# Optimization experiments

Hardware: AMD Instinct MI355X
Metric: run time of the kernel (lower is better)

Reference implementation:

```python
import jax, jax.numpy as jnp
import numpy as np
import math

DIM_K = 64  # head dim used for scaling
NEG = -1000000000.0

def setup_inputs() -> dict:
    key = jax.random.key(0)
    k1, k2, k3, k4 = jax.random.split(key, 4)
    B, H, S, D = 4, 16, 2048, 64
    return {
        "key": jax.random.normal(k1, (B, H, S, D), dtype=jnp.float32),
        "query": jax.random.normal(k2, (B, H, S, D), dtype=jnp.float32),
        "value": jax.random.normal(k3, (B, H, S, D), dtype=jnp.float32),
        "mask": jax.random.randint(k4, (B, S, S), 0, 2, dtype=jnp.int32),
    }

def reference(key, query, value, mask):
    # scores: [B,H,Sq,Sk]
    scores = jnp.einsum('bhqd,bhkd->bhqk', query, key) / math.sqrt(DIM_K)
    scores = jnp.where(mask[:, None, :, :] == 0, NEG, scores)
    attn = jax.nn.softmax(scores, axis=-1)  # dropout is identity in eval mode
    return jnp.einsum('bhqk,bhkd->bhqd', attn, value)
```

## Files before the change

kernel.cpp:

```cpp
#include <hip/hip_runtime.h>
#include <hip/hip_bf16.h>
#include <stdint.h>

#define B_ 4
#define H_ 16
#define S_ 2048
#define D_ 64
#define NKT (S_ / 64)
#define QM 128

typedef __attribute__((ext_vector_type(8))) short bf16x8;
typedef __attribute__((ext_vector_type(4))) float f32x4;
typedef unsigned long long u64;
typedef unsigned int u32;

__device__ inline short f2bf(float f) {
  union { float f; u32 u; } x; x.f = f;
  u32 r = x.u + 0x7FFFu + ((x.u >> 16) & 1u);
  return (short)(r >> 16);
}
__device__ inline short4 f2bf4(float4 v) {
  short4 s; s.x = f2bf(v.x); s.y = f2bf(v.y); s.z = f2bf(v.z); s.w = f2bf(v.w);
  return s;
}

__device__ inline int SW(int row, int byteoff) {
  return row * 128 + (byteoff ^ ((row & 7) << 4));
}

__device__ inline void gll16(const void* g, void* l) {
  __builtin_amdgcn_global_load_lds(
      (const __attribute__((address_space(1))) u32*)g,
      (__attribute__((address_space(3))) u32*)(uintptr_t)l, 16, 0, 0);
}

__global__ __launch_bounds__(256)
void prepass(const float* __restrict__ Kg, const float* __restrict__ Vg,
             const int* __restrict__ Mg,
             char* __restrict__ Ksw, char* __restrict__ Vsw, u64* __restrict__ Mp) {
  __shared__ short tile[4096];
  const int bid = blockIdx.x, tid = threadIdx.x;
  if (bid < 8192) {
    int idx = bid * 256 + tid;
    int row = idx >> 4, c4 = idx & 15;
    float4 v = *(const float4*)(Kg + (size_t)idx * 4);
    *(short4*)(Ksw + (size_t)row * 128 + ((c4 * 8) ^ ((row & 7) << 4))) = f2bf4(v);
  } else if (bid < 10240) {
    int vb = bid - 8192;
    char* ct = (char*)tile;
    int c4 = tid & 15, g = tid >> 4;
    const float* src = Vg + (size_t)vb * (64 * D_) + (size_t)(g * 4) * D_ + c4 * 4;
    float4 vv[4];
#pragma unroll
    for (int i = 0; i < 4; ++i) vv[i] = *(const float4*)(src + (size_t)i * D_);
    const float* vf = (const float*)vv;
#pragma unroll
    for (int dd = 0; dd < 4; ++dd) {
      short4 s;
      s.x = f2bf(vf[0 * 4 + dd]);
      s.y = f2bf(vf[1 * 4 + dd]);
      s.z = f2bf(vf[2 * 4 + dd]);
      s.w = f2bf(vf[3 * 4 + dd]);
      *(short4*)(ct + SW(c4 * 4 + dd, g * 8)) = s;
    }
    __syncthreads();
    char* dst = Vsw + (size_t)vb * 8192;
#pragma unroll
    for (int j = 0; j < 2; ++j)
      *(float4*)(dst + tid * 16 + j * 4096) = *(const float4*)(ct + tid * 16 + j * 4096);
  } else {
    int pb = bid - 10240;
    int gbase = pb * 1024;
#pragma unroll
    for (int j = 0; j < 4; ++j) {
      int idx = gbase + j * 256 + tid;
      u64 bits = __ballot(Mg[idx] != 0);
      if ((tid & 63) == 0) Mp[idx >> 6] = bits;
    }
  }
}

__global__ __launch_bounds__(256, 4)
void attn_kernel(const float* __restrict__ Qg,
                 const char* __restrict__ Ksw,
                 const char* __restrict__ Vsw,
                 const u64* __restrict__ Mp,
                 float* __restrict__ Og) {
  __shared__ short sK[2][4096];
  __shared__ short sV[2][4096];

  const int tid  = threadIdx.x;
  const int w    = tid >> 6;
  const int lane = tid & 63;
  const int quad = lane >> 4;
  const int c    = lane & 15;
  const int bh   = blockIdx.y;
  const int b    = bh >> 4;
  const int q0   = blockIdx.x * QM;
  const size_t base = (size_t)bh * (S_ * D_);
  const char* Kt = Ksw + (size_t)bh * (S_ * 128);
  const char* Vt = Vsw + (size_t)bh * (S_ * 128);
  char* cK0 = (char*)sK;

  const float SC = 0.125f * 1.44269504088896f;
#pragma unroll
  for (int j = 0; j < 8; ++j) {
    int idx = tid + j * 256;
    int row = idx >> 4, c4 = idx & 15;
    float4 v = *(const float4*)(Qg + base + (size_t)(q0 + row) * D_ + c4 * 4);
    v.x *= SC; v.y *= SC; v.z *= SC; v.w *= SC;
    *(short4*)(cK0 + SW(row, c4 * 8)) = f2bf4(v);
  }
  __syncthreads();
  bf16x8 qa[2][2];
#pragma unroll
  for (int gi = 0; gi < 2; ++gi) {
    qa[gi][0] = *(bf16x8*)(cK0 + SW(32 * w + 16 * gi + c, quad * 16));
    qa[gi][1] = *(bf16x8*)(cK0 + SW(32 * w + 16 * gi + c, 64 + quad * 16));
  }
  __syncthreads();

#pragma unroll
  for (int j = 0; j < 2; ++j) {
    gll16(Kt + tid * 16 + j * 4096, (char*)sK[0] + tid * 16 + j * 4096);
    gll16(Vt + tid * 16 + j * 4096, (char*)sV[0] + tid * 16 + j * 4096);
  }

  f32x4 acco[2][4];
  float l_part[2] = {0.f, 0.f};
#pragma unroll
  for (int gi = 0; gi < 2; ++gi)
#pragma unroll
    for (int i = 0; i < 4; ++i) acco[gi][i] = f32x4{0, 0, 0, 0};

  const u64* mrowp = Mp + ((size_t)b * S_ + q0 + 32 * w + c) * NKT;

  for (int kt = 0; kt < NKT; ++kt) {
    const char* cK = (const char*)sK[kt & 1];
    const char* cV = (const char*)sV[kt & 1];

    __syncthreads();

    u64 mw[2];
    mw[0] = mrowp[kt];
    mw[1] = mrowp[16 * NKT + kt];

    f32x4 accs[2][4];
#pragma unroll
    for (int n = 0; n < 4; ++n) {
      bf16x8 kb0 = *(bf16x8*)(cK + SW(16 * n + c, quad * 16));
      bf16x8 kb1 = *(bf16x8*)(cK + SW(16 * n + c, 64 + quad * 16));
#pragma unroll
      for (int gi = 0; gi < 2; ++gi) {
        f32x4 z = {0, 0, 0, 0};
        z = __builtin_amdgcn_mfma_f32_16x16x32_bf16(kb0, qa[gi][0], z, 0, 0, 0);
        z = __builtin_amdgcn_mfma_f32_16x16x32_bf16(kb1, qa[gi][1], z, 0, 0, 0);
        accs[gi][n] = z;
      }
    }

    if (kt + 1 < NKT) {
      char* kn = (char*)sK[(kt + 1) & 1];
      char* vn = (char*)sV[(kt + 1) & 1];
      const char* kg = Kt + (size_t)(kt + 1) * 8192;
      const char* vg = Vt + (size_t)(kt + 1) * 8192;
#pragma unroll
      for (int j = 0; j < 2; ++j) {
        gll16(kg + tid * 16 + j * 4096, kn + tid * 16 + j * 4096);
        gll16(vg + tid * 16 + j * 4096, vn + tid * 16 + j * 4096);
      }
    }

    bf16x8 pa[2][2];
#pragma unroll
    for (int gi = 0; gi < 2; ++gi) {
      u32 mlo = (u32)(mw[gi] >> (4 * quad));
      u32 mhi = (u32)(mw[gi] >> (4 * quad + 32));
      float e[4][4];
#pragma unroll
      for (int n = 0; n < 4; ++n) {
        u32 mword = (n < 2) ? mlo : mhi;
        int sh = 16 * (n & 1);
#pragma unroll
        for (int r = 0; r < 4; ++r)
          e[n][r] = ((mword >> (sh + r)) & 1u) ? exp2f(accs[gi][n][r]) : 0.0f;
      }
      l_part[gi] += ((e[0][0] + e[0][1]) + (e[0][2] + e[0][3]))
                  + ((e[1][0] + e[1][1]) + (e[1][2] + e[1][3]))
                  + ((e[2][0] + e[2][1]) + (e[2][2] + e[2][3]))
                  + ((e[3][0] + e[3][1]) + (e[3][2] + e[3][3]));

      u32 pk[4][2];
#pragma unroll
      for (int n = 0; n < 4; ++n) {
        union { __hip_bfloat162 h; u32 u; } p0, p1;
        p0.h = __float22bfloat162_rn(make_float2(e[n][0], e[n][1]));
        p1.h = __float22bfloat162_rn(make_float2(e[n][2], e[n][3]));
        pk[n][0] = p0.u;
        pk[n][1] = p1.u;
      }

#pragma unroll
      for (int t = 0; t < 2; ++t) {
        union { bf16x8 v; u32 uw[4]; } pu;
#pragma unroll
        for (int h = 0; h < 2; ++h) {
          u32 a  = pk[2 * t][h];
          u32 bq = pk[2 * t + 1][h];
          asm("v_permlane32_swap_b32 %0, %1" : "+v"(a), "+v"(bq));
          asm("v_permlane16_swap_b32 %0, %1" : "+v"(a), "+v"(bq));
          pu.uw[h]     = a;
          pu.uw[2 + h] = bq;
        }
        pa[gi][t] = pu.v;
      }
    }

#pragma unroll
    for (int dn = 0; dn < 4; ++dn) {
      bf16x8 vb0 = *(bf16x8*)(cV + SW(16 * dn + c, quad * 16));
      bf16x8 vb1 = *(bf16x8*)(cV + SW(16 * dn + c, 64 + quad * 16));
#pragma unroll
      for (int gi = 0; gi < 2; ++gi) {
        acco[gi][dn] = __builtin_amdgcn_mfma_f32_16x16x32_bf16(pa[gi][0], vb0, acco[gi][dn], 0, 0, 0);
        acco[gi][dn] = __builtin_amdgcn_mfma_f32_16x16x32_bf16(pa[gi][1], vb1, acco[gi][dn], 0, 0, 0);
      }
    }
  }

#pragma unroll
  for (int gi = 0; gi < 2; ++gi) {
    float l = l_part[gi];
    l += __shfl_xor(l, 16);
    l += __shfl_xor(l, 32);
    float inv = 1.0f / l;
#pragma unroll
    for (int r = 0; r < 4; ++r) {
      float invr = __shfl(inv, (lane & 48) | (quad * 4 + r));
      size_t orow = base + (size_t)(q0 + 32 * w + 16 * gi + quad * 4 + r) * D_;
#pragma unroll
      for (int dn = 0; dn < 4; ++dn)
        Og[orow + 16 * dn + c] = acco[gi][dn][r] * invr;
    }
  }
}

extern "C" void kernel_launch(void* const* d_in, const int* in_sizes, int n_in,
                              void* d_out, int out_size, void* d_ws, size_t ws_size,
                              hipStream_t stream) {
  const float* Kg = (const float*)d_in[0];
  const float* Qg = (const float*)d_in[1];
  const float* Vg = (const float*)d_in[2];
  const int*   Mg = (const int*)d_in[3];
  float* Og = (float*)d_out;

  char* ws  = (char*)d_ws;
  u64*  Mp  = (u64*)ws;
  char* Ksw = ws + (size_t)(2u << 20);
  char* Vsw = ws + (size_t)(2u << 20) + (16u << 20);

  prepass<<<26624, 256, 0, stream>>>(Kg, Vg, Mg, Ksw, Vsw, Mp);
  attn_kernel<<<dim3(S_ / QM, B_ * H_), 256, 0, stream>>>(Qg, Ksw, Vsw, Mp, Og);
}
```

Before: 320.4 us.

## Use packed bf16 converts, MFMA row sums, block swizzle, setprio, and precomputed LDS offsets

Replaces the software bf16 rounding with the hardware v_cvt_pk_bf16_f32 instruction in the prepass and the Q load. The attention loop is unrolled by two so LDS buffer offsets become constants, and per-lane swizzle offsets are computed once. The softmax denominator is now accumulated with extra MFMAs against a ones vector, which drops the scalar adds and the cross-lane shuffles at the end. Masking now feeds -1000 into exp2f instead of using a select around it, s_setprio is raised around MFMA blocks, and a block-index remap groups eight heads per query tile to change L2 locality. The row sum is taken over bf16-rounded probabilities, which slightly changes numerics.

Result: faster. 302.4 us (-5.6%).

```diff
diff --git a/kernel.cpp b/kernel.cpp
--- a/kernel.cpp
+++ b/kernel.cpp
@@ -14,14 +14,10 @@
 typedef unsigned long long u64;
 typedef unsigned int u32;
 
-__device__ inline short f2bf(float f) {
-  union { float f; u32 u; } x; x.f = f;
-  u32 r = x.u + 0x7FFFu + ((x.u >> 16) & 1u);
-  return (short)(r >> 16);
-}
-__device__ inline short4 f2bf4(float4 v) {
-  short4 s; s.x = f2bf(v.x); s.y = f2bf(v.y); s.z = f2bf(v.z); s.w = f2bf(v.w);
-  return s;
+__device__ inline u32 cvt_pk_bf16(float lo, float hi) {
+  u32 r;
+  asm("v_cvt_pk_bf16_f32 %0, %1, %2" : "=v"(r) : "v"(lo), "v"(hi));
+  return r;
 }
 
 __device__ inline int SW(int row, int byteoff) {
@@ -44,7 +40,10 @@
     int idx = bid * 256 + tid;
     int row = idx >> 4, c4 = idx & 15;
     float4 v = *(const float4*)(Kg + (size_t)idx * 4);
-    *(short4*)(Ksw + (size_t)row * 128 + ((c4 * 8) ^ ((row & 7) << 4))) = f2bf4(v);
+    uint2 u;
+    u.x = cvt_pk_bf16(v.x, v.y);
+    u.y = cvt_pk_bf16(v.z, v.w);
+    *(uint2*)(Ksw + (size_t)row * 128 + ((c4 * 8) ^ ((row & 7) << 4))) = u;
   } else if (bid < 10240) {
     int vb = bid - 8192;
     char* ct = (char*)tile;
@@ -56,12 +55,10 @@
     const float* vf = (const float*)vv;
 #pragma unroll
     for (int dd = 0; dd < 4; ++dd) {
-      short4 s;
-      s.x = f2bf(vf[0 * 4 + dd]);
-      s.y = f2bf(vf[1 * 4 + dd]);
-      s.z = f2bf(vf[2 * 4 + dd]);
-      s.w = f2bf(vf[3 * 4 + dd]);
-      *(short4*)(ct + SW(c4 * 4 + dd, g * 8)) = s;
+      uint2 u;
+      u.x = cvt_pk_bf16(vf[0 * 4 + dd], vf[1 * 4 + dd]);
+      u.y = cvt_pk_bf16(vf[2 * 4 + dd], vf[3 * 4 + dd]);
+      *(uint2*)(ct + SW(c4 * 4 + dd, g * 8)) = u;
     }
     __syncthreads();
     char* dst = Vsw + (size_t)vb * 8192;
@@ -94,9 +91,12 @@
   const int lane = tid & 63;
   const int quad = lane >> 4;
   const int c    = lane & 15;
-  const int bh   = blockIdx.y;
+
+  const int flat = blockIdx.x + (int)gridDim.x * blockIdx.y;
+  const int bh   = (flat & 7) | ((flat >> 7) << 3);
+  const int q0   = ((flat >> 3) & 15) * QM;
   const int b    = bh >> 4;
-  const int q0   = blockIdx.x * QM;
+
   const size_t base = (size_t)bh * (S_ * D_);
   const char* Kt = Ksw + (size_t)bh * (S_ * 128);
   const char* Vt = Vsw + (size_t)bh * (S_ * 128);
@@ -108,8 +108,10 @@
     int idx = tid + j * 256;
     int row = idx >> 4, c4 = idx & 15;
     float4 v = *(const float4*)(Qg + base + (size_t)(q0 + row) * D_ + c4 * 4);
-    v.x *= SC; v.y *= SC; v.z *= SC; v.w *= SC;
-    *(short4*)(cK0 + SW(row, c4 * 8)) = f2bf4(v);
+    uint2 u;
+    u.x = cvt_pk_bf16(v.x * SC, v.y * SC);
+    u.y = cvt_pk_bf16(v.z * SC, v.w * SC);
+    *(uint2*)(cK0 + SW(row, c4 * 8)) = u;
   }
   __syncthreads();
   bf16x8 qa[2][2];
@@ -126,121 +128,139 @@
     gll16(Vt + tid * 16 + j * 4096, (char*)sV[0] + tid * 16 + j * 4096);
   }
 
+  int koff[4][2];
+#pragma unroll
+  for (int n = 0; n < 4; ++n) {
+    koff[n][0] = SW(16 * n + c, quad * 16);
+    koff[n][1] = SW(16 * n + c, 64 + quad * 16);
+  }
+
+  bf16x8 ones;
+#pragma unroll
+  for (int i = 0; i < 8; ++i) ones[i] = (short)0x3F80;
+
   f32x4 acco[2][4];
-  float l_part[2] = {0.f, 0.f};
-#pragma unroll
-  for (int gi = 0; gi < 2; ++gi)
+  f32x4 acc_l[2];
+#pragma unroll
+  for (int gi = 0; gi < 2; ++gi) {
+    acc_l[gi] = f32x4{0, 0, 0, 0};
 #pragma unroll
     for (int i = 0; i < 4; ++i) acco[gi][i] = f32x4{0, 0, 0, 0};
+  }
 
   const u64* mrowp = Mp + ((size_t)b * S_ + q0 + 32 * w + c) * NKT;
 
-  for (int kt = 0; kt < NKT; ++kt) {
-    const char* cK = (const char*)sK[kt & 1];
-    const char* cV = (const char*)sV[kt & 1];
-
-    __syncthreads();
-
-    u64 mw[2];
-    mw[0] = mrowp[kt];
-    mw[1] = mrowp[16 * NKT + kt];
-
-    f32x4 accs[2][4];
-#pragma unroll
-    for (int n = 0; n < 4; ++n) {
-      bf16x8 kb0 = *(bf16x8*)(cK + SW(16 * n + c, quad * 16));
-      bf16x8 kb1 = *(bf16x8*)(cK + SW(16 * n + c, 64 + quad * 16));
+  const char* kbase = (const char*)sK;
+  const char* vbase = (const char*)sV;
+
+  for (int kt2 = 0; kt2 < NKT; kt2 += 2) {
+#pragma unroll
+    for (int p = 0; p < 2; ++p) {
+      const int kt = kt2 + p;
+
+      __syncthreads();
+
+      u64 mw[2];
+      mw[0] = mrowp[kt];
+      mw[1] = mrowp[16 * NKT + kt];
+
+      f32x4 accs[2][4];
+      __builtin_amdgcn_s_setprio(1);
+#pragma unroll
+      for (int n = 0; n < 4; ++n) {
+        bf16x8 kb0 = *(bf16x8*)(kbase + koff[n][0] + p * 8192);
+        bf16x8 kb1 = *(bf16x8*)(kbase + koff[n][1] + p * 8192);
+#pragma unroll
+        for (int gi = 0; gi < 2; ++gi) {
+          f32x4 z = {0, 0, 0, 0};
+          z = __builtin_amdgcn_mfma_f32_16x16x32_bf16(kb0, qa[gi][0], z, 0, 0, 0);
+          z = __builtin_amdgcn_mfma_f32_16x16x32_bf16(kb1, qa[gi][1], z, 0, 0, 0);
+          accs[gi][n] = z;
+        }
+      }
+      __builtin_amdgcn_s_setprio(0);
+
+      if (kt + 1 < NKT) {
+        char* kn = (char*)sK + (p ^ 1) * 8192;
+        char* vn = (char*)sV + (p ^ 1) * 8192;
+        const char* kg = Kt + (size_t)(kt + 1) * 8192;
+        const char* vg = Vt + (size_t)(kt + 1) * 8192;
+#pragma unroll
+        for (int j = 0; j < 2; ++j) {
+          gll16(kg + tid * 16 + j * 4096, kn + tid * 16 + j * 4096);
+          gll16(vg + tid * 16 + j * 4096, vn + tid * 16 + j * 4096);
+        }
+      }
+
+      bf16x8 pa[2][2];
 #pragma unroll
       for (int gi = 0; gi < 2; ++gi) {
-        f32x4 z = {0, 0, 0, 0};
-        z = __builtin_amdgcn_mfma_f32_16x16x32_bf16(kb0, qa[gi][0], z, 0, 0, 0);
-        z = __builtin_amdgcn_mfma_f32_16x16x32_bf16(kb1, qa[gi][1], z, 0, 0, 0);
-        accs[gi][n] = z;
-      }
-    }
-
-    if (kt + 1 < NKT) {
-      char* kn = (char*)sK[(kt + 1) & 1];
-      char* vn = (char*)sV[(kt + 1) & 1];
-      const char* kg = Kt + (size_t)(kt + 1) * 8192;
-      const char* vg = Vt + (size_t)(kt + 1) * 8192;
-#pragma unroll
-      for (int j = 0; j < 2; ++j) {
-        gll16(kg + tid * 16 + j * 4096, kn + tid * 16 + j * 4096);
-        gll16(vg + tid * 16 + j * 4096, vn + tid * 16 + j * 4096);
-      }
-    }
-
-    bf16x8 pa[2][2];
-#pragma unroll
-    for (int gi = 0; gi < 2; ++gi) {
-      u32 mlo = (u32)(mw[gi] >> (4 * quad));
-      u32 mhi = (u32)(mw[gi] >> (4 * quad + 32));
-      float e[4][4];
-#pragma unroll
-      for (int n = 0; n < 4; ++n) {
-        u32 mword = (n < 2) ? mlo : mhi;
-        int sh = 16 * (n & 1);
-#pragma unroll
-        for (int r = 0; r < 4; ++r)
-          e[n][r] = ((mword >> (sh + r)) & 1u) ? exp2f(accs[gi][n][r]) : 0.0f;
-      }
-      l_part[gi] += ((e[0][0] + e[0][1]) + (e[0][2] + e[0][3]))
-                  + ((e[1][0] + e[1][1]) + (e[1][2] + e[1][3]))
-                  + ((e[2][0] + e[2][1]) + (e[2][2] + e[2][3]))
-                  + ((e[3][0] + e[3][1]) + (e[3][2] + e[3][3]));
-
-      u32 pk[4][2];
-#pragma unroll
-      for (int n = 0; n < 4; ++n) {
-        union { __hip_bfloat162 h; u32 u; } p0, p1;
-        p0.h = __float22bfloat162_rn(make_float2(e[n][0], e[n][1]));
-        p1.h = __float22bfloat162_rn(make_float2(e[n][2], e[n][3]));
-        pk[n][0] = p0.u;
-        pk[n][1] = p1.u;
-      }
-
-#pragma unroll
-      for (int t = 0; t < 2; ++t) {
-        union { bf16x8 v; u32 uw[4]; } pu;
-#pragma unroll
-        for (int h = 0; h < 2; ++h) {
-          u32 a  = pk[2 * t][h];
-          u32 bq = pk[2 * t + 1][h];
-          asm("v_permlane32_swap_b32 %0, %1" : "+v"(a), "+v"(bq));
-          asm("v_permlane16_swap_b32 %0, %1" : "+v"(a), "+v"(bq));
-          pu.uw[h]     = a;
-          pu.uw[2 + h] = bq;
-        }
-        pa[gi][t] = pu.v;
-      }
-    }
-
-#pragma unroll
-    for (int dn = 0; dn < 4; ++dn) {
-      bf16x8 vb0 = *(bf16x8*)(cV + SW(16 * dn + c, quad * 16));
-      bf16x8 vb1 = *(bf16x8*)(cV + SW(16 * dn + c, 64 + quad * 16));
+        u32 mlo = (u32)(mw[gi] >> (4 * quad));
+        u32 mhi = (u32)(mw[gi] >> (4 * quad + 32));
+        float e[4][4];
+#pragma unroll
+        for (int n = 0; n < 4; ++n) {
+          u32 mword = (n < 2) ? mlo : mhi;
+          int sh = 16 * (n & 1);
+#pragma unroll
+          for (int r = 0; r < 4; ++r) {
+            float sm = ((mword >> (sh + r)) & 1u) ? accs[gi][n][r] : -1000.0f;
+            e[n][r] = exp2f(sm);
+          }
+        }
+
+        u32 pk[4][2];
+#pragma unroll
+        for (int n = 0; n < 4; ++n) {
+          pk[n][0] = cvt_pk_bf16(e[n][0], e[n][1]);
+          pk[n][1] = cvt_pk_bf16(e[n][2], e[n][3]);
+        }
+
+#pragma unroll
+        for (int t = 0; t < 2; ++t) {
+          union { bf16x8 v; u32 uw[4]; } pu;
+#pragma unroll
+          for (int h = 0; h < 2; ++h) {
+            u32 a  = pk[2 * t][h];
+            u32 bq = pk[2 * t + 1][h];
+            asm("v_permlane32_swap_b32 %0, %1" : "+v"(a), "+v"(bq));
+            asm("v_permlane16_swap_b32 %0, %1" : "+v"(a), "+v"(bq));
+            pu.uw[h]     = a;
+            pu.uw[2 + h] = bq;
+          }
+          pa[gi][t] = pu.v;
+        }
+      }
+
+      __builtin_amdgcn_s_setprio(1);
+#pragma unroll
+      for (int dn = 0; dn < 4; ++dn) {
+        bf16x8 vb0 = *(bf16x8*)(vbase + koff[dn][0] + p * 8192);
+        bf16x8 vb1 = *(bf16x8*)(vbase + koff[dn][1] + p * 8192);
+#pragma unroll
+        for (int gi = 0; gi < 2; ++gi) {
+          acco[gi][dn] = __builtin_amdgcn_mfma_f32_16x16x32_bf16(pa[gi][0], vb0, acco[gi][dn], 0, 0, 0);
+          acco[gi][dn] = __builtin_amdgcn_mfma_f32_16x16x32_bf16(pa[gi][1], vb1, acco[gi][dn], 0, 0, 0);
+        }
+      }
 #pragma unroll
       for (int gi = 0; gi < 2; ++gi) {
-        acco[gi][dn] = __builtin_amdgcn_mfma_f32_16x16x32_bf16(pa[gi][0], vb0, acco[gi][dn], 0, 0, 0);
-        acco[gi][dn] = __builtin_amdgcn_mfma_f32_16x16x32_bf16(pa[gi][1], vb1, acco[gi][dn], 0, 0, 0);
-      }
+        acc_l[gi] = __builtin_amdgcn_mfma_f32_16x16x32_bf16(pa[gi][0], ones, acc_l[gi], 0, 0, 0);
+        acc_l[gi] = __builtin_amdgcn_mfma_f32_16x16x32_bf16(pa[gi][1], ones, acc_l[gi], 0, 0, 0);
+      }
+      __builtin_amdgcn_s_setprio(0);
     }
   }
 
 #pragma unroll
   for (int gi = 0; gi < 2; ++gi) {
-    float l = l_part[gi];
-    l += __shfl_xor(l, 16);
-    l += __shfl_xor(l, 32);
-    float inv = 1.0f / l;
 #pragma unroll
     for (int r = 0; r < 4; ++r) {
-      float invr = __shfl(inv, (lane & 48) | (quad * 4 + r));
+      float inv = 1.0f / acc_l[gi][r];
       size_t orow = base + (size_t)(q0 + 32 * w + 16 * gi + quad * 4 + r) * D_;
 #pragma unroll
       for (int dn = 0; dn < 4; ++dn)
-        Og[orow + 16 * dn + c] = acco[gi][dn][r] * invr;
+        Og[orow + 16 * dn + c] = acco[gi][dn][r] * inv;
     }
   }
 }
```
